# Performance work log

Measured on AMD Instinct MI355X. Metric: run time of the kernel, lower is better.

Reference implementation:

```python
import jax, jax.numpy as jnp
import numpy as np

N = 50000       # nodes
E = 800000      # edges (avg degree 16)
C_IN = 128
C_HID = 64
C_OUT = 64
NEG_SLOPE = 0.2  # PyG GATConv default


def setup_inputs() -> dict:
    key = jax.random.key(0)
    ks = jax.random.split(key, 20)
    inp = {
        "x": jax.random.normal(ks[0], (N, C_IN), dtype=jnp.float32),
        "edge_index": jax.random.randint(ks[1], (2, E), 0, N, dtype=jnp.int32),
        "batch_size": N,
        "framework": 1,
    }
    dims = [(C_IN, C_HID), (C_HID, C_HID), (C_HID, C_OUT)]
    k = 2
    for i, (cin, cout) in enumerate(dims):
        s = 1.0 / np.sqrt(cin)
        inp[f"W{i}"] = jax.random.normal(ks[k], (cin, cout), jnp.float32) * s; k += 1
        inp[f"a_src{i}"] = jax.random.normal(ks[k], (cout,), jnp.float32) * (1.0 / np.sqrt(cout)); k += 1
        inp[f"a_dst{i}"] = jax.random.normal(ks[k], (cout,), jnp.float32) * (1.0 / np.sqrt(cout)); k += 1
        inp[f"b{i}"] = jnp.zeros((cout,), jnp.float32); k += 1
    return inp


def _gat_conv(h, src, dst, n, W, a_src, a_dst, b):
    # h: [n, cin] -> [n, cout]; single head, PyG GATConv semantics
    hp = h @ W                                   # [n, cout]
    alpha_s = hp @ a_src                         # [n]
    alpha_d = hp @ a_dst                         # [n]
    e = alpha_s[src] + alpha_d[dst]              # [E'] per-edge logits
    e = jnp.where(e > 0, e, NEG_SLOPE * e)       # leaky_relu(0.2)
    # segment softmax over incoming edges of each destination node
    m = jax.ops.segment_max(e, dst, num_segments=n)
    e = jnp.exp(e - m[dst])
    denom = jax.ops.segment_sum(e, dst, num_segments=n)
    a = e / (denom[dst] + 1e-16)                 # [E']
    msg = hp[src] * a[:, None]                   # [E', cout]
    out = jax.ops.segment_sum(msg, dst, num_segments=n)
    return out + b


def reference(x, edge_index, batch_size, framework,
              W0, a_src0, a_dst0, b0,
              W1, a_src1, a_dst1, b1,
              W2, a_src2, a_dst2, b2):
    n = x.shape[0]
    loops = jnp.arange(n, dtype=edge_index.dtype)  # PyG add_self_loops=True
    src = jnp.concatenate([edge_index[0], loops])
    dst = jnp.concatenate([edge_index[1], loops])
    params = [(W0, a_src0, a_dst0, b0), (W1, a_src1, a_dst1, b1), (W2, a_src2, a_dst2, b2)]
    h = x
    for W, a_s, a_d, b in params:
        h = jax.nn.relu(_gat_conv(h, src, dst, n, W, a_s, a_d, b))
    if framework:
        return h
    return h[:batch_size]
```

## Files before the change

kernel.cpp:

```cpp
#include <hip/hip_runtime.h>
#include <hip/hip_fp16.h>
#include <math.h>

#define NEG_SLOPE 0.2f
#define BSHIFT 8
#define BCAP 8192

typedef __attribute__((ext_vector_type(8))) short bf16x8;
typedef __attribute__((ext_vector_type(4))) float f32x4;

__device__ __forceinline__ float leaky(float e) {
    return e > 0.f ? e : NEG_SLOPE * e;
}
__device__ __forceinline__ float to_f(float x) { return x; }
__device__ __forceinline__ float to_f(__half x) { return __half2float(x); }


__global__ __launch_bounds__(256) void partition_kernel(
        const int* __restrict__ src, const int* __restrict__ dst,
        int* __restrict__ bucketLen, int* __restrict__ pairs, int E, int nbk) {
    __shared__ int cnt[256];
    __shared__ int run[256];
    int t = threadIdx.x;
    int chunk = (E + gridDim.x - 1) / gridDim.x;
    int beg = blockIdx.x * chunk;
    int end = min(beg + chunk, E);
    cnt[t] = 0;
    __syncthreads();
    for (int i = beg + t; i < end; i += 256)
        atomicAdd(&cnt[dst[i] >> BSHIFT], 1);
    __syncthreads();
    if (t < nbk) run[t] = t * BCAP + atomicAdd(&bucketLen[t], cnt[t]);
    __syncthreads();
    for (int i = beg + t; i < end; i += 256) {
        int d = dst[i];
        int slot = atomicAdd(&run[d >> BSHIFT], 1);
        if (slot < (d >> BSHIFT) * BCAP + BCAP)
            pairs[slot] = (src[i] << BSHIFT) | (d & 255);
    }
}

__device__ void csr_build_body(
        int b, const int* __restrict__ bucketLen, const int* __restrict__ pairs,
        int* __restrict__ off, int* __restrict__ degA,
        int* __restrict__ csr_src, int N) {
    __shared__ int degl[256];
    __shared__ int s[256];
    __shared__ int cur[256];
    int t = threadIdx.x;
    int n0 = b << BSHIFT;
    int nodecnt = min(256, N - n0);
    int ebeg = b * BCAP;
    int eend = ebeg + bucketLen[b];

    degl[t] = 0;
    __syncthreads();
    for (int i = ebeg + t; i < eend; i += 256)
        atomicAdd(&degl[pairs[i] & 255], 1);
    __syncthreads();

    int v = degl[t];
    s[t] = v;
    __syncthreads();
    for (int o = 1; o < 256; o <<= 1) {
        int x = (t >= o) ? s[t - o] : 0;
        __syncthreads();
        s[t] += x;
        __syncthreads();
    }
    int excl = s[t] - v;
    if (t < nodecnt) {
        off[n0 + t] = ebeg + excl;
        degA[n0 + t] = v;
    }
    cur[t] = excl;
    __syncthreads();

    for (int i = ebeg + t; i < eend; i += 256) {
        int pk = pairs[i];
        int p = atomicAdd(&cur[pk & 255], 1);
        csr_src[ebeg + p] = pk >> BSHIFT;
    }
}


__device__ __forceinline__ unsigned f2bf_bits(float x) {
    unsigned u = __float_as_uint(x);
    return (u + 0x7fffu + ((u >> 16) & 1u)) >> 16;
}

__global__ __launch_bounds__(256) void pack_w3_kernel(
        const float* __restrict__ W0, const float* __restrict__ W1,
        const float* __restrict__ W2, short* __restrict__ Whi,
        short* __restrict__ Wlo, int* __restrict__ bucketLen) {
    int idx = blockIdx.x * 256 + threadIdx.x;
    if (idx < 256) bucketLen[idx] = 0;
    if (idx >= 16384) return;
    const float* W;
    int base, li;
    if (idx < 8192)       { W = W0; base = 0;     li = idx; }
    else if (idx < 12288) { W = W1; base = 8192;  li = idx - 8192; }
    else                  { W = W2; base = 12288; li = idx - 12288; }
    int k = li >> 6, col = li & 63;
    int c = k >> 5, kin = k & 31;
    int g = col >> 4, nn = col & 15;
    float x = W[li];
    unsigned hb = f2bf_bits(x);
    float hf = __uint_as_float(hb << 16);
    unsigned lb = f2bf_bits(x - hf);
    int o = base + (((c * 4 + g) * 16 + nn) << 5) + kin;
    Whi[o] = (short)hb;
    Wlo[o] = (short)lb;
}


template <int CIN, typename InT>
__device__ void gemm_body(
        int bid, const InT* __restrict__ h, const short* __restrict__ Whi,
        const short* __restrict__ Wlo,
        const float* __restrict__ a_src, const float* __restrict__ a_dst,
        __half* __restrict__ hp, float* __restrict__ as_, float* __restrict__ ad_,
        int n) {
    constexpr int KC = CIN / 32;
    int t = threadIdx.x, wave = t >> 6, lane = t & 63;
    int quad = lane >> 4, l16 = lane & 15;
    int node0 = bid * 64 + wave * 16;

    f32x4 acc[4];
#pragma unroll
    for (int g = 0; g < 4; ++g) acc[g] = (f32x4){0.f, 0.f, 0.f, 0.f};

    int nodeA = node0 + l16;
    bool va = nodeA < n;
    const InT* hrow = h + (size_t)(va ? nodeA : 0) * CIN + quad * 8;

#pragma unroll
    for (int c = 0; c < KC; ++c) {
        bf16x8 bhi[4], blo[4];
#pragma unroll
        for (int g = 0; g < 4; ++g) {
            int o = (((c * 4 + g) * 16 + l16) << 5) + quad * 8;
            bhi[g] = *(const bf16x8*)(Whi + o);
            blo[g] = *(const bf16x8*)(Wlo + o);
        }
        bf16x8 ahi, alo;
#pragma unroll
        for (int j = 0; j < 8; ++j) {
            float x = va ? to_f(hrow[c * 32 + j]) : 0.f;
            unsigned hb = f2bf_bits(x);
            float hf = __uint_as_float(hb << 16);
            unsigned lb = f2bf_bits(x - hf);
            ahi[j] = (short)hb;
            alo[j] = (short)lb;
        }
#pragma unroll
        for (int g = 0; g < 4; ++g) {
            acc[g] = __builtin_amdgcn_mfma_f32_16x16x32_bf16(ahi, bhi[g], acc[g], 0, 0, 0);
            acc[g] = __builtin_amdgcn_mfma_f32_16x16x32_bf16(ahi, blo[g], acc[g], 0, 0, 0);
            acc[g] = __builtin_amdgcn_mfma_f32_16x16x32_bf16(alo, bhi[g], acc[g], 0, 0, 0);
        }
    }

    float as4[4], ad4[4];
#pragma unroll
    for (int g = 0; g < 4; ++g) {
        as4[g] = a_src[g * 16 + l16];
        ad4[g] = a_dst[g * 16 + l16];
    }
#pragma unroll
    for (int r = 0; r < 4; ++r) {
        int node = node0 + quad * 4 + r;
        bool v = node < n;
        float vs = 0.f, vd = 0.f;
#pragma unroll
        for (int g = 0; g < 4; ++g) {
            float val = acc[g][r];
            if (v) hp[(size_t)node * 64 + g * 16 + l16] = __float2half_rn(val);
            vs = fmaf(val, as4[g], vs);
            vd = fmaf(val, ad4[g], vd);
        }
#pragma unroll
        for (int o = 1; o <= 8; o <<= 1) {
            vs += __shfl_xor(vs, o);
            vd += __shfl_xor(vd, o);
        }
        if (v && l16 == 0) {
            as_[node] = vs;
            ad_[node] = vd;
        }
    }
}

__global__ __launch_bounds__(256) void csr_gemm0_kernel(
        const int* __restrict__ bucketLen, const int* __restrict__ pairs,
        int* __restrict__ off, int* __restrict__ degA, int* __restrict__ csr_src,
        int N, int nbk,
        const float* __restrict__ x, const short* __restrict__ Whi,
        const short* __restrict__ Wlo, const float* __restrict__ a_src,
        const float* __restrict__ a_dst, __half* __restrict__ hp,
        float* __restrict__ as_, float* __restrict__ ad_) {
    if ((int)blockIdx.x < nbk)
        csr_build_body(blockIdx.x, bucketLen, pairs, off, degA, csr_src, N);
    else
        gemm_body<128, float>((int)blockIdx.x - nbk, x, Whi, Wlo, a_src, a_dst,
                              hp, as_, ad_, N);
}

template <int CIN, typename InT>
__global__ __launch_bounds__(256) void gemm_mfma_kernel(
        const InT* __restrict__ h, const short* __restrict__ Whi,
        const short* __restrict__ Wlo,
        const float* __restrict__ a_src, const float* __restrict__ a_dst,
        __half* __restrict__ hp, float* __restrict__ as_, float* __restrict__ ad_,
        int n) {
    gemm_body<CIN, InT>((int)blockIdx.x, h, Whi, Wlo, a_src, a_dst, hp, as_, ad_, n);
}


__device__ __forceinline__ void h4_to_f(uint2 u, float* f) {
    __half2 a = *(__half2*)&u.x;
    __half2 b = *(__half2*)&u.y;
    float2 f01 = __half22float2(a);
    float2 f23 = __half22float2(b);
    f[0] = f01.x; f[1] = f01.y; f[2] = f23.x; f[3] = f23.y;
}

__device__ __forceinline__ void store_row(float* out, size_t idx, float4 r) {
    ((float4*)out)[idx] = r;
}
__device__ __forceinline__ void store_row(__half* out, size_t idx, float4 r) {
    __half2 a = __floats2half2_rn(r.x, r.y);
    __half2 b = __floats2half2_rn(r.z, r.w);
    uint2 u;
    u.x = *(unsigned*)&a;
    u.y = *(unsigned*)&b;
    ((uint2*)out)[idx] = u;
}
__device__ __forceinline__ void store_el(float* out, size_t idx, float v) { out[idx] = v; }
__device__ __forceinline__ void store_el(__half* out, size_t idx, float v) { out[idx] = __float2half_rn(v); }

template <typename OutT>
__global__ __launch_bounds__(256) void agg_kernel(
        const __half* __restrict__ hp,
        const float* __restrict__ as_, const float* __restrict__ ad_,
        const int* __restrict__ off, const int* __restrict__ degA,
        const int* __restrict__ csr_src,
        const float* __restrict__ bias, OutT* __restrict__ out, int n) {
    __shared__ float pw[4][64];
    __shared__ int ps[4][64];
    int t = threadIdx.x;
    int wave = t >> 6, lane = t & 63;
    int hf = lane >> 5, l32 = lane & 31;
    int node = blockIdx.x * 8 + wave * 2 + hf;
    if (node >= n) return;

    int beg = off[node];
    int deg = degA[node];
    int end = beg + deg;
    float adst = ad_[node];
    float e_self = leaky(as_[node] + adst);

    if (deg <= 32) {
        bool valid = l32 < deg;
        int s = valid ? csr_src[beg + l32] : 0;
        float e = valid ? leaky(as_[s] + adst) : -3.4e38f;

        float m = e;
#pragma unroll
        for (int o = 16; o > 0; o >>= 1) m = fmaxf(m, __shfl_xor(m, o));
        m = fmaxf(m, e_self);

        float p = valid ? __expf(e - m) : 0.f;
        float pself = __expf(e_self - m);
        float se = p;
#pragma unroll
        for (int o = 16; o > 0; o >>= 1) se += __shfl_xor(se, o);
        se += pself;
        float inv = 1.0f / (se + 1e-16f);
        p *= inv;

        pw[wave][lane] = p;
        ps[wave][lane] = s;

        int group = l32 >> 4, sub = l32 & 15;
        const uint2* hp2 = (const uint2*)hp;

        float wself = (group == 0) ? pself * inv : 0.f;
        float hv[4];
        h4_to_f(hp2[(size_t)node * 16 + sub], hv);
        float ax = wself * hv[0], ay = wself * hv[1];
        float az = wself * hv[2], aw = wself * hv[3];

        int base = hf * 32;
        for (int j = group; j < deg; j += 8) {
            float w4[4];
            uint2 u4[4];
#pragma unroll
            for (int q = 0; q < 4; ++q) {
                int jj = j + 2 * q;
                bool ok = jj < deg;
                w4[q] = ok ? pw[wave][base + jj] : 0.f;
                u4[q] = ok ? hp2[(size_t)ps[wave][base + jj] * 16 + sub]
                           : make_uint2(0u, 0u);
            }
#pragma unroll
            for (int q = 0; q < 4; ++q) {
                float f[4];
                h4_to_f(u4[q], f);
                ax = fmaf(w4[q], f[0], ax);
                ay = fmaf(w4[q], f[1], ay);
                az = fmaf(w4[q], f[2], az);
                aw = fmaf(w4[q], f[3], aw);
            }
        }

        ax += __shfl_xor(ax, 16);
        ay += __shfl_xor(ay, 16);
        az += __shfl_xor(az, 16);
        aw += __shfl_xor(aw, 16);

        float4 b4 = ((const float4*)bias)[sub];
        float4 r;
        r.x = ax + b4.x; r.x = r.x > 0.f ? r.x : 0.f;
        r.y = ay + b4.y; r.y = r.y > 0.f ? r.y : 0.f;
        r.z = az + b4.z; r.z = r.z > 0.f ? r.z : 0.f;
        r.w = aw + b4.w; r.w = r.w > 0.f ? r.w : 0.f;
        if (group == 0) store_row(out, (size_t)node * 16 + sub, r);
    } else {
        float mymax = e_self;
        for (int i = beg + l32; i < end; i += 32) {
            int s = csr_src[i];
            mymax = fmaxf(mymax, leaky(as_[s] + adst));
        }
#pragma unroll
        for (int o = 16; o > 0; o >>= 1) mymax = fmaxf(mymax, __shfl_xor(mymax, o));
        float m = mymax;

        float se = 0.f;
        for (int i = beg + l32; i < end; i += 32) {
            int s = csr_src[i];
            se += __expf(leaky(as_[s] + adst) - m);
        }
#pragma unroll
        for (int o = 16; o > 0; o >>= 1) se += __shfl_xor(se, o);
        se += __expf(e_self - m);
        float inv = 1.0f / (se + 1e-16f);

        const __half2* hpx = (const __half2*)hp;
        float2 hs = __half22float2(hpx[(size_t)node * 32 + l32]);
        float wself = __expf(e_self - m) * inv;
        float a0 = wself * hs.x, a1 = wself * hs.y;
        for (int i = beg; i < end; ++i) {
            int s = csr_src[i];
            float w = __expf(leaky(as_[s] + adst) - m) * inv;
            float2 hv = __half22float2(hpx[(size_t)s * 32 + l32]);
            a0 = fmaf(w, hv.x, a0);
            a1 = fmaf(w, hv.y, a1);
        }
        float r0 = a0 + bias[l32 * 2];
        float r1 = a1 + bias[l32 * 2 + 1];
        store_el(out, (size_t)node * 64 + l32 * 2,     r0 > 0.f ? r0 : 0.f);
        store_el(out, (size_t)node * 64 + l32 * 2 + 1, r1 > 0.f ? r1 : 0.f);
    }
}


extern "C" void kernel_launch(void* const* d_in, const int* in_sizes, int n_in,
                              void* d_out, int out_size, void* d_ws, size_t ws_size,
                              hipStream_t stream) {
    const float* x = (const float*)d_in[0];
    const int* edge_index = (const int*)d_in[1];
    const int N = in_sizes[0] / 128;
    const int E = in_sizes[1] / 2;
    const int NBK = (N + 255) >> BSHIFT;

    const float* W[3]    = {(const float*)d_in[4], (const float*)d_in[8],  (const float*)d_in[12]};
    const float* asrc[3] = {(const float*)d_in[5], (const float*)d_in[9],  (const float*)d_in[13]};
    const float* adst[3] = {(const float*)d_in[6], (const float*)d_in[10], (const float*)d_in[14]};
    const float* bias[3] = {(const float*)d_in[7], (const float*)d_in[11], (const float*)d_in[15]};

    char* ws = (char*)d_ws;
    size_t o = 0;
    auto alloc = [&](size_t bytes) {
        char* p = ws + o;
        o += (bytes + 255) & ~(size_t)255;
        return p;
    };
    int* bucketLen    = (int*)alloc(256 * 4);
    int* pairs        = (int*)alloc((size_t)NBK * BCAP * 4);
    int* off          = (int*)alloc((size_t)N * 4);
    int* degA         = (int*)alloc((size_t)N * 4);
    int* csr_src      = (int*)alloc((size_t)NBK * BCAP * 4);
    float* as_        = (float*)alloc((size_t)N * 4);
    float* ad_        = (float*)alloc((size_t)N * 4);
    __half* hpbuf     = (__half*)alloc((size_t)N * 64 * 2);
    __half* actB      = (__half*)alloc((size_t)N * 64 * 2);
    short* Whi        = (short*)alloc(16384 * 2);
    short* Wlo        = (short*)alloc(16384 * 2);

    const int* srcp = edge_index;
    const int* dstp = edge_index + E;

    int gb = (N + 63) / 64;
    int ab = (N + 7) / 8;

    pack_w3_kernel<<<64, 256, 0, stream>>>(W[0], W[1], W[2], Whi, Wlo, bucketLen);
    partition_kernel<<<1024, 256, 0, stream>>>(srcp, dstp, bucketLen, pairs, E, NBK);

    csr_gemm0_kernel<<<NBK + gb, 256, 0, stream>>>(
        bucketLen, pairs, off, degA, csr_src, N, NBK,
        x, Whi, Wlo, asrc[0], adst[0], hpbuf, as_, ad_);
    agg_kernel<__half><<<ab, 256, 0, stream>>>(
        hpbuf, as_, ad_, off, degA, csr_src, bias[0], actB, N);

    gemm_mfma_kernel<64, __half><<<gb, 256, 0, stream>>>(
        actB, Whi + 8192, Wlo + 8192, asrc[1], adst[1], hpbuf, as_, ad_, N);
    agg_kernel<__half><<<ab, 256, 0, stream>>>(
        hpbuf, as_, ad_, off, degA, csr_src, bias[1], actB, N);

    gemm_mfma_kernel<64, __half><<<gb, 256, 0, stream>>>(
        actB, Whi + 12288, Wlo + 12288, asrc[2], adst[2], hpbuf, as_, ad_, N);
    agg_kernel<float><<<ab, 256, 0, stream>>>(
        hpbuf, as_, ad_, off, degA, csr_src, bias[2], (float*)d_out, N);
}
```

Baseline: 273.0 us.

## Fuse all GAT stages into one cooperative persistent kernel with grid syncs

```diff
diff --git a/kernel.cpp b/kernel.cpp
--- a/kernel.cpp
+++ b/kernel.cpp
@@ -1,6 +1,9 @@
 #include <hip/hip_runtime.h>
 #include <hip/hip_fp16.h>
+#include <hip/hip_cooperative_groups.h>
 #include <math.h>
+
+namespace cg = cooperative_groups;
 
 #define NEG_SLOPE 0.2f
 #define BSHIFT 8
@@ -15,87 +18,16 @@
 __device__ __forceinline__ float to_f(float x) { return x; }
 __device__ __forceinline__ float to_f(__half x) { return __half2float(x); }
 
-
-__global__ __launch_bounds__(256) void partition_kernel(
-        const int* __restrict__ src, const int* __restrict__ dst,
-        int* __restrict__ bucketLen, int* __restrict__ pairs, int E, int nbk) {
-    __shared__ int cnt[256];
-    __shared__ int run[256];
-    int t = threadIdx.x;
-    int chunk = (E + gridDim.x - 1) / gridDim.x;
-    int beg = blockIdx.x * chunk;
-    int end = min(beg + chunk, E);
-    cnt[t] = 0;
-    __syncthreads();
-    for (int i = beg + t; i < end; i += 256)
-        atomicAdd(&cnt[dst[i] >> BSHIFT], 1);
-    __syncthreads();
-    if (t < nbk) run[t] = t * BCAP + atomicAdd(&bucketLen[t], cnt[t]);
-    __syncthreads();
-    for (int i = beg + t; i < end; i += 256) {
-        int d = dst[i];
-        int slot = atomicAdd(&run[d >> BSHIFT], 1);
-        if (slot < (d >> BSHIFT) * BCAP + BCAP)
-            pairs[slot] = (src[i] << BSHIFT) | (d & 255);
-    }
-}
-
-__device__ void csr_build_body(
-        int b, const int* __restrict__ bucketLen, const int* __restrict__ pairs,
-        int* __restrict__ off, int* __restrict__ degA,
-        int* __restrict__ csr_src, int N) {
-    __shared__ int degl[256];
-    __shared__ int s[256];
-    __shared__ int cur[256];
-    int t = threadIdx.x;
-    int n0 = b << BSHIFT;
-    int nodecnt = min(256, N - n0);
-    int ebeg = b * BCAP;
-    int eend = ebeg + bucketLen[b];
-
-    degl[t] = 0;
-    __syncthreads();
-    for (int i = ebeg + t; i < eend; i += 256)
-        atomicAdd(&degl[pairs[i] & 255], 1);
-    __syncthreads();
-
-    int v = degl[t];
-    s[t] = v;
-    __syncthreads();
-    for (int o = 1; o < 256; o <<= 1) {
-        int x = (t >= o) ? s[t - o] : 0;
-        __syncthreads();
-        s[t] += x;
-        __syncthreads();
-    }
-    int excl = s[t] - v;
-    if (t < nodecnt) {
-        off[n0 + t] = ebeg + excl;
-        degA[n0 + t] = v;
-    }
-    cur[t] = excl;
-    __syncthreads();
-
-    for (int i = ebeg + t; i < eend; i += 256) {
-        int pk = pairs[i];
-        int p = atomicAdd(&cur[pk & 255], 1);
-        csr_src[ebeg + p] = pk >> BSHIFT;
-    }
-}
-
-
 __device__ __forceinline__ unsigned f2bf_bits(float x) {
     unsigned u = __float_as_uint(x);
     return (u + 0x7fffu + ((u >> 16) & 1u)) >> 16;
 }
 
-__global__ __launch_bounds__(256) void pack_w3_kernel(
-        const float* __restrict__ W0, const float* __restrict__ W1,
+
+__device__ __forceinline__ void pack_body(
+        int idx, const float* __restrict__ W0, const float* __restrict__ W1,
         const float* __restrict__ W2, short* __restrict__ Whi,
-        short* __restrict__ Wlo, int* __restrict__ bucketLen) {
-    int idx = blockIdx.x * 256 + threadIdx.x;
-    if (idx < 256) bucketLen[idx] = 0;
-    if (idx >= 16384) return;
+        short* __restrict__ Wlo) {
     const float* W;
     int base, li;
     if (idx < 8192)       { W = W0; base = 0;     li = idx; }
@@ -114,6 +46,76 @@
 }
 
 
+__device__ void partition_body(
+        const int* __restrict__ src, const int* __restrict__ dst,
+        int* __restrict__ bucketLen, int* __restrict__ pairs, int E, int nbk) {
+    __shared__ int cnt[256];
+    __shared__ int run[256];
+    int t = threadIdx.x;
+    int nblk = gridDim.x;
+    int chunk = (E + nblk - 1) / nblk;
+    int beg = blockIdx.x * chunk;
+    int end = min(beg + chunk, E);
+    cnt[t] = 0;
+    __syncthreads();
+    for (int i = beg + t; i < end; i += 256)
+        atomicAdd(&cnt[dst[i] >> BSHIFT], 1);
+    __syncthreads();
+    if (t < nbk) run[t] = t * BCAP + atomicAdd(&bucketLen[t], cnt[t]);
+    __syncthreads();
+    for (int i = beg + t; i < end; i += 256) {
+        int d = dst[i];
+        int slot = atomicAdd(&run[d >> BSHIFT], 1);
+        if (slot < (d >> BSHIFT) * BCAP + BCAP)
+            pairs[slot] = (src[i] << BSHIFT) | (d & 255);
+    }
+}
+
+__device__ void csr_build_body(
+        int b, const int* __restrict__ bucketLen, const int* __restrict__ pairs,
+        int* __restrict__ off, int* __restrict__ degA,
+        int* __restrict__ csr_src, int N) {
+    __shared__ int degl[256];
+    __shared__ int s[256];
+    __shared__ int cur[256];
+    int t = threadIdx.x;
+    int n0 = b << BSHIFT;
+    int nodecnt = min(256, N - n0);
+    int ebeg = b * BCAP;
+    int eend = ebeg + bucketLen[b];
+
+    degl[t] = 0;
+    __syncthreads();
+    for (int i = ebeg + t; i < eend; i += 256)
+        atomicAdd(&degl[pairs[i] & 255], 1);
+    __syncthreads();
+
+    int v = degl[t];
+    s[t] = v;
+    __syncthreads();
+    for (int o = 1; o < 256; o <<= 1) {
+        int x = (t >= o) ? s[t - o] : 0;
+        __syncthreads();
+        s[t] += x;
+        __syncthreads();
+    }
+    int excl = s[t] - v;
+    if (t < nodecnt) {
+        off[n0 + t] = ebeg + excl;
+        degA[n0 + t] = v;
+    }
+    cur[t] = excl;
+    __syncthreads();
+
+    for (int i = ebeg + t; i < eend; i += 256) {
+        int pk = pairs[i];
+        int p = atomicAdd(&cur[pk & 255], 1);
+        csr_src[ebeg + p] = pk >> BSHIFT;
+    }
+    __syncthreads();
+}
+
+
 template <int CIN, typename InT>
 __device__ void gemm_body(
         int bid, const InT* __restrict__ h, const short* __restrict__ Whi,
@@ -189,6 +191,233 @@
             ad_[node] = vd;
         }
     }
+}
+
+
+__device__ __forceinline__ void h4_to_f(uint2 u, float* f) {
+    __half2 a = *(__half2*)&u.x;
+    __half2 b = *(__half2*)&u.y;
+    float2 f01 = __half22float2(a);
+    float2 f23 = __half22float2(b);
+    f[0] = f01.x; f[1] = f01.y; f[2] = f23.x; f[3] = f23.y;
+}
+
+__device__ __forceinline__ void store_row(float* out, size_t idx, float4 r) {
+    ((float4*)out)[idx] = r;
+}
+__device__ __forceinline__ void store_row(__half* out, size_t idx, float4 r) {
+    __half2 a = __floats2half2_rn(r.x, r.y);
+    __half2 b = __floats2half2_rn(r.z, r.w);
+    uint2 u;
+    u.x = *(unsigned*)&a;
+    u.y = *(unsigned*)&b;
+    ((uint2*)out)[idx] = u;
+}
+__device__ __forceinline__ void store_el(float* out, size_t idx, float v) { out[idx] = v; }
+__device__ __forceinline__ void store_el(__half* out, size_t idx, float v) { out[idx] = __float2half_rn(v); }
+
+template <typename OutT>
+__device__ void agg_body(
+        int g0, const __half* __restrict__ hp,
+        const float* __restrict__ as_, const float* __restrict__ ad_,
+        const int* __restrict__ off, const int* __restrict__ degA,
+        const int* __restrict__ csr_src,
+        const float* __restrict__ bias, OutT* __restrict__ out, int n) {
+    __shared__ float pw[4][64];
+    __shared__ int ps[4][64];
+    int t = threadIdx.x;
+    int wave = t >> 6, lane = t & 63;
+    int hf = lane >> 5, l32 = lane & 31;
+    int node = g0 * 8 + wave * 2 + hf;
+    if (node < n) {
+        int beg = off[node];
+        int deg = degA[node];
+        int end = beg + deg;
+        float adst = ad_[node];
+        float e_self = leaky(as_[node] + adst);
+
+        if (deg <= 32) {
+            bool valid = l32 < deg;
+            int s = valid ? csr_src[beg + l32] : 0;
+            float e = valid ? leaky(as_[s] + adst) : -3.4e38f;
+
+            float m = e;
+#pragma unroll
+            for (int o = 16; o > 0; o >>= 1) m = fmaxf(m, __shfl_xor(m, o));
+            m = fmaxf(m, e_self);
+
+            float p = valid ? __expf(e - m) : 0.f;
+            float pself = __expf(e_self - m);
+            float se = p;
+#pragma unroll
+            for (int o = 16; o > 0; o >>= 1) se += __shfl_xor(se, o);
+            se += pself;
+            float inv = 1.0f / (se + 1e-16f);
+            p *= inv;
+
+            pw[wave][lane] = p;
+            ps[wave][lane] = s;
+
+            int group = l32 >> 4, sub = l32 & 15;
+            const uint2* hp2 = (const uint2*)hp;
+
+            float wself = (group == 0) ? pself * inv : 0.f;
+            float hv[4];
+            h4_to_f(hp2[(size_t)node * 16 + sub], hv);
+            float ax = wself * hv[0], ay = wself * hv[1];
+            float az = wself * hv[2], aw = wself * hv[3];
+
+            int base = hf * 32;
+            for (int j = group; j < deg; j += 8) {
+                float w4[4];
+                uint2 u4[4];
+#pragma unroll
+                for (int q = 0; q < 4; ++q) {
+                    int jj = j + 2 * q;
+                    bool ok = jj < deg;
+                    w4[q] = ok ? pw[wave][base + jj] : 0.f;
+                    u4[q] = ok ? hp2[(size_t)ps[wave][base + jj] * 16 + sub]
+                               : make_uint2(0u, 0u);
+                }
+#pragma unroll
+                for (int q = 0; q < 4; ++q) {
+                    float f[4];
+                    h4_to_f(u4[q], f);
+                    ax = fmaf(w4[q], f[0], ax);
+                    ay = fmaf(w4[q], f[1], ay);
+                    az = fmaf(w4[q], f[2], az);
+                    aw = fmaf(w4[q], f[3], aw);
+                }
+            }
+
+            ax += __shfl_xor(ax, 16);
+            ay += __shfl_xor(ay, 16);
+            az += __shfl_xor(az, 16);
+            aw += __shfl_xor(aw, 16);
+
+            float4 b4 = ((const float4*)bias)[sub];
+            float4 r;
+            r.x = ax + b4.x; r.x = r.x > 0.f ? r.x : 0.f;
+            r.y = ay + b4.y; r.y = r.y > 0.f ? r.y : 0.f;
+            r.z = az + b4.z; r.z = r.z > 0.f ? r.z : 0.f;
+            r.w = aw + b4.w; r.w = r.w > 0.f ? r.w : 0.f;
+            if (group == 0) store_row(out, (size_t)node * 16 + sub, r);
+        } else {
+            float mymax = e_self;
+            for (int i = beg + l32; i < end; i += 32) {
+                int s = csr_src[i];
+                mymax = fmaxf(mymax, leaky(as_[s] + adst));
+            }
+#pragma unroll
+            for (int o = 16; o > 0; o >>= 1) mymax = fmaxf(mymax, __shfl_xor(mymax, o));
+            float m = mymax;
+
+            float se = 0.f;
+            for (int i = beg + l32; i < end; i += 32) {
+                int s = csr_src[i];
+                se += __expf(leaky(as_[s] + adst) - m);
+            }
+#pragma unroll
+            for (int o = 16; o > 0; o >>= 1) se += __shfl_xor(se, o);
+            se += __expf(e_self - m);
+            float inv = 1.0f / (se + 1e-16f);
+
+            const __half2* hpx = (const __half2*)hp;
+            float2 hs = __half22float2(hpx[(size_t)node * 32 + l32]);
+            float wself = __expf(e_self - m) * inv;
+            float a0 = wself * hs.x, a1 = wself * hs.y;
+            for (int i = beg; i < end; ++i) {
+                int s = csr_src[i];
+                float w = __expf(leaky(as_[s] + adst) - m) * inv;
+                float2 hv = __half22float2(hpx[(size_t)s * 32 + l32]);
+                a0 = fmaf(w, hv.x, a0);
+                a1 = fmaf(w, hv.y, a1);
+            }
+            float r0 = a0 + bias[l32 * 2];
+            float r1 = a1 + bias[l32 * 2 + 1];
+            store_el(out, (size_t)node * 64 + l32 * 2,     r0 > 0.f ? r0 : 0.f);
+            store_el(out, (size_t)node * 64 + l32 * 2 + 1, r1 > 0.f ? r1 : 0.f);
+        }
+    }
+}
+
+
+struct MegaArgs {
+    const float* x;
+    const int* src;
+    const int* dst;
+    const float* W0; const float* W1; const float* W2;
+    const float* as0; const float* ad0; const float* b0;
+    const float* as1; const float* ad1; const float* b1;
+    const float* as2; const float* ad2; const float* b2;
+    int* bucketLen; int* pairs; int* off; int* degA; int* csr_src;
+    float* asA; float* adA;
+    __half* hp; __half* actB;
+    short* Whi; short* Wlo;
+    float* out;
+    int N, E, NBK, GB, AB;
+};
+
+__global__ __launch_bounds__(256) void mega_kernel(MegaArgs a) {
+    cg::grid_group grid = cg::this_grid();
+    int bid = blockIdx.x, nblk = gridDim.x, t = threadIdx.x;
+
+    for (int idx = bid * 256 + t; idx < 16384; idx += nblk * 256)
+        pack_body(idx, a.W0, a.W1, a.W2, a.Whi, a.Wlo);
+    if (bid == 0) a.bucketLen[t] = 0;
+    grid.sync();
+
+    partition_body(a.src, a.dst, a.bucketLen, a.pairs, a.E, a.NBK);
+    grid.sync();
+
+    if (bid < a.NBK) {
+        csr_build_body(bid, a.bucketLen, a.pairs, a.off, a.degA, a.csr_src, a.N);
+    } else {
+        for (int tile = bid - a.NBK; tile < a.GB; tile += nblk - a.NBK)
+            gemm_body<128, float>(tile, a.x, a.Whi, a.Wlo, a.as0, a.ad0,
+                                  a.hp, a.asA, a.adA, a.N);
+    }
+    grid.sync();
+
+    for (int g = bid; g < a.AB; g += nblk)
+        agg_body<__half>(g, a.hp, a.asA, a.adA, a.off, a.degA, a.csr_src,
+                         a.b0, a.actB, a.N);
+    grid.sync();
+
+    for (int tile = bid; tile < a.GB; tile += nblk)
+        gemm_body<64, __half>(tile, a.actB, a.Whi + 8192, a.Wlo + 8192,
+                              a.as1, a.ad1, a.hp, a.asA, a.adA, a.N);
+    grid.sync();
+
+    for (int g = bid; g < a.AB; g += nblk)
+        agg_body<__half>(g, a.hp, a.asA, a.adA, a.off, a.degA, a.csr_src,
+                         a.b1, a.actB, a.N);
+    grid.sync();
+
+    for (int tile = bid; tile < a.GB; tile += nblk)
+        gemm_body<64, __half>(tile, a.actB, a.Whi + 12288, a.Wlo + 12288,
+                              a.as2, a.ad2, a.hp, a.asA, a.adA, a.N);
+    grid.sync();
+
+    for (int g = bid; g < a.AB; g += nblk)
+        agg_body<float>(g, a.hp, a.asA, a.adA, a.off, a.degA, a.csr_src,
+                        a.b2, a.out, a.N);
+}
+
+
+__global__ __launch_bounds__(256) void pack_w3_kernel(
+        const float* __restrict__ W0, const float* __restrict__ W1,
+        const float* __restrict__ W2, short* __restrict__ Whi,
+        short* __restrict__ Wlo, int* __restrict__ bucketLen) {
+    int idx = blockIdx.x * 256 + threadIdx.x;
+    if (idx < 256) bucketLen[idx] = 0;
+    if (idx < 16384) pack_body(idx, W0, W1, W2, Whi, Wlo);
+}
+
+__global__ __launch_bounds__(256) void partition_kernel(
+        const int* __restrict__ src, const int* __restrict__ dst,
+        int* __restrict__ bucketLen, int* __restrict__ pairs, int E, int nbk) {
+    partition_body(src, dst, bucketLen, pairs, E, nbk);
 }
 
 __global__ __launch_bounds__(256) void csr_gemm0_kernel(
@@ -216,29 +445,6 @@
     gemm_body<CIN, InT>((int)blockIdx.x, h, Whi, Wlo, a_src, a_dst, hp, as_, ad_, n);
 }
 
-
-__device__ __forceinline__ void h4_to_f(uint2 u, float* f) {
-    __half2 a = *(__half2*)&u.x;
-    __half2 b = *(__half2*)&u.y;
-    float2 f01 = __half22float2(a);
-    float2 f23 = __half22float2(b);
-    f[0] = f01.x; f[1] = f01.y; f[2] = f23.x; f[3] = f23.y;
-}
-
-__device__ __forceinline__ void store_row(float* out, size_t idx, float4 r) {
-    ((float4*)out)[idx] = r;
-}
-__device__ __forceinline__ void store_row(__half* out, size_t idx, float4 r) {
-    __half2 a = __floats2half2_rn(r.x, r.y);
-    __half2 b = __floats2half2_rn(r.z, r.w);
-    uint2 u;
-    u.x = *(unsigned*)&a;
-    u.y = *(unsigned*)&b;
-    ((uint2*)out)[idx] = u;
-}
-__device__ __forceinline__ void store_el(float* out, size_t idx, float v) { out[idx] = v; }
-__device__ __forceinline__ void store_el(__half* out, size_t idx, float v) { out[idx] = __float2half_rn(v); }
-
 template <typename OutT>
 __global__ __launch_bounds__(256) void agg_kernel(
         const __half* __restrict__ hp,
@@ -246,122 +452,7 @@
         const int* __restrict__ off, const int* __restrict__ degA,
         const int* __restrict__ csr_src,
         const float* __restrict__ bias, OutT* __restrict__ out, int n) {
-    __shared__ float pw[4][64];
-    __shared__ int ps[4][64];
-    int t = threadIdx.x;
-    int wave = t >> 6, lane = t & 63;
-    int hf = lane >> 5, l32 = lane & 31;
-    int node = blockIdx.x * 8 + wave * 2 + hf;
-    if (node >= n) return;
-
-    int beg = off[node];
-    int deg = degA[node];
-    int end = beg + deg;
-    float adst = ad_[node];
-    float e_self = leaky(as_[node] + adst);
-
-    if (deg <= 32) {
-        bool valid = l32 < deg;
-        int s = valid ? csr_src[beg + l32] : 0;
-        float e = valid ? leaky(as_[s] + adst) : -3.4e38f;
-
-        float m = e;
-#pragma unroll
-        for (int o = 16; o > 0; o >>= 1) m = fmaxf(m, __shfl_xor(m, o));
-        m = fmaxf(m, e_self);
-
-        float p = valid ? __expf(e - m) : 0.f;
-        float pself = __expf(e_self - m);
-        float se = p;
-#pragma unroll
-        for (int o = 16; o > 0; o >>= 1) se += __shfl_xor(se, o);
-        se += pself;
-        float inv = 1.0f / (se + 1e-16f);
-        p *= inv;
-
-        pw[wave][lane] = p;
-        ps[wave][lane] = s;
-
-        int group = l32 >> 4, sub = l32 & 15;
-        const uint2* hp2 = (const uint2*)hp;
-
-        float wself = (group == 0) ? pself * inv : 0.f;
-        float hv[4];
-        h4_to_f(hp2[(size_t)node * 16 + sub], hv);
-        float ax = wself * hv[0], ay = wself * hv[1];
-        float az = wself * hv[2], aw = wself * hv[3];
-
-        int base = hf * 32;
-        for (int j = group; j < deg; j += 8) {
-            float w4[4];
-            uint2 u4[4];
-#pragma unroll
-            for (int q = 0; q < 4; ++q) {
-                int jj = j + 2 * q;
-                bool ok = jj < deg;
-                w4[q] = ok ? pw[wave][base + jj] : 0.f;
-                u4[q] = ok ? hp2[(size_t)ps[wave][base + jj] * 16 + sub]
-                           : make_uint2(0u, 0u);
-            }
-#pragma unroll
-            for (int q = 0; q < 4; ++q) {
-                float f[4];
-                h4_to_f(u4[q], f);
-                ax = fmaf(w4[q], f[0], ax);
-                ay = fmaf(w4[q], f[1], ay);
-                az = fmaf(w4[q], f[2], az);
-                aw = fmaf(w4[q], f[3], aw);
-            }
-        }
-
-        ax += __shfl_xor(ax, 16);
-        ay += __shfl_xor(ay, 16);
-        az += __shfl_xor(az, 16);
-        aw += __shfl_xor(aw, 16);
-
-        float4 b4 = ((const float4*)bias)[sub];
-        float4 r;
-        r.x = ax + b4.x; r.x = r.x > 0.f ? r.x : 0.f;
-        r.y = ay + b4.y; r.y = r.y > 0.f ? r.y : 0.f;
-        r.z = az + b4.z; r.z = r.z > 0.f ? r.z : 0.f;
-        r.w = aw + b4.w; r.w = r.w > 0.f ? r.w : 0.f;
-        if (group == 0) store_row(out, (size_t)node * 16 + sub, r);
-    } else {
-        float mymax = e_self;
-        for (int i = beg + l32; i < end; i += 32) {
-            int s = csr_src[i];
-            mymax = fmaxf(mymax, leaky(as_[s] + adst));
-        }
-#pragma unroll
-        for (int o = 16; o > 0; o >>= 1) mymax = fmaxf(mymax, __shfl_xor(mymax, o));
-        float m = mymax;
-
-        float se = 0.f;
-        for (int i = beg + l32; i < end; i += 32) {
-            int s = csr_src[i];
-            se += __expf(leaky(as_[s] + adst) - m);
-        }
-#pragma unroll
-        for (int o = 16; o > 0; o >>= 1) se += __shfl_xor(se, o);
-        se += __expf(e_self - m);
-        float inv = 1.0f / (se + 1e-16f);
-
-        const __half2* hpx = (const __half2*)hp;
-        float2 hs = __half22float2(hpx[(size_t)node * 32 + l32]);
-        float wself = __expf(e_self - m) * inv;
-        float a0 = wself * hs.x, a1 = wself * hs.y;
-        for (int i = beg; i < end; ++i) {
-            int s = csr_src[i];
-            float w = __expf(leaky(as_[s] + adst) - m) * inv;
-            float2 hv = __half22float2(hpx[(size_t)s * 32 + l32]);
-            a0 = fmaf(w, hv.x, a0);
-            a1 = fmaf(w, hv.y, a1);
-        }
-        float r0 = a0 + bias[l32 * 2];
-        float r1 = a1 + bias[l32 * 2 + 1];
-        store_el(out, (size_t)node * 64 + l32 * 2,     r0 > 0.f ? r0 : 0.f);
-        store_el(out, (size_t)node * 64 + l32 * 2 + 1, r1 > 0.f ? r1 : 0.f);
-    }
+    agg_body<OutT>((int)blockIdx.x, hp, as_, ad_, off, degA, csr_src, bias, out, n);
 }
 
 
@@ -404,22 +495,68 @@
     int gb = (N + 63) / 64;
     int ab = (N + 7) / 8;
 
-    pack_w3_kernel<<<64, 256, 0, stream>>>(W[0], W[1], W[2], Whi, Wlo, bucketLen);
-    partition_kernel<<<1024, 256, 0, stream>>>(srcp, dstp, bucketLen, pairs, E, NBK);
-
-    csr_gemm0_kernel<<<NBK + gb, 256, 0, stream>>>(
-        bucketLen, pairs, off, degA, csr_src, N, NBK,
-        x, Whi, Wlo, asrc[0], adst[0], hpbuf, as_, ad_);
-    agg_kernel<__half><<<ab, 256, 0, stream>>>(
-        hpbuf, as_, ad_, off, degA, csr_src, bias[0], actB, N);
-
-    gemm_mfma_kernel<64, __half><<<gb, 256, 0, stream>>>(
-        actB, Whi + 8192, Wlo + 8192, asrc[1], adst[1], hpbuf, as_, ad_, N);
-    agg_kernel<__half><<<ab, 256, 0, stream>>>(
-        hpbuf, as_, ad_, off, degA, csr_src, bias[1], actB, N);
-
-    gemm_mfma_kernel<64, __half><<<gb, 256, 0, stream>>>(
-        actB, Whi + 12288, Wlo + 12288, asrc[2], adst[2], hpbuf, as_, ad_, N);
-    agg_kernel<float><<<ab, 256, 0, stream>>>(
-        hpbuf, as_, ad_, off, degA, csr_src, bias[2], (float*)d_out, N);
-}
+    static int s_blocks = 0;
+    static bool s_coop_ok = true;
+    if (s_coop_ok && s_blocks == 0) {
+        int dev = 0;
+        hipDeviceProp_t prop;
+        if (hipGetDevice(&dev) == hipSuccess &&
+            hipGetDeviceProperties(&prop, dev) == hipSuccess &&
+            prop.cooperativeLaunch) {
+            int maxPerCU = 0;
+            if (hipOccupancyMaxActiveBlocksPerMultiprocessor(
+                    &maxPerCU, mega_kernel, 256, 0) == hipSuccess && maxPerCU > 0) {
+                long b = (long)prop.multiProcessorCount * (long)maxPerCU;
+                if (b > 4096) b = 4096;
+                s_blocks = (int)b;
+            } else {
+                s_coop_ok = false;
+            }
+        } else {
+            s_coop_ok = false;
+        }
+    }
+
+    bool launched = false;
+    if (s_coop_ok && s_blocks > NBK) {
+        MegaArgs a;
+        a.x = x; a.src = srcp; a.dst = dstp;
+        a.W0 = W[0]; a.W1 = W[1]; a.W2 = W[2];
+        a.as0 = asrc[0]; a.ad0 = adst[0]; a.b0 = bias[0];
+        a.as1 = asrc[1]; a.ad1 = adst[1]; a.b1 = bias[1];
+        a.as2 = asrc[2]; a.ad2 = adst[2]; a.b2 = bias[2];
+        a.bucketLen = bucketLen; a.pairs = pairs; a.off = off;
+        a.degA = degA; a.csr_src = csr_src;
+        a.asA = as_; a.adA = ad_;
+        a.hp = hpbuf; a.actB = actB;
+        a.Whi = Whi; a.Wlo = Wlo;
+        a.out = (float*)d_out;
+        a.N = N; a.E = E; a.NBK = NBK; a.GB = gb; a.AB = ab;
+        void* params[] = { (void*)&a };
+        hipError_t err = hipLaunchCooperativeKernel(
+            mega_kernel, dim3(s_blocks), dim3(256), params, 0u, stream);
+        if (err == hipSuccess) {
+            launched = true;
+        } else {
+            s_coop_ok = false;
+        }
+    }
+
+    if (!launched) {
+        pack_w3_kernel<<<64, 256, 0, stream>>>(W[0], W[1], W[2], Whi, Wlo, bucketLen);
+        partition_kernel<<<1024, 256, 0, stream>>>(srcp, dstp, bucketLen, pairs, E, NBK);
+        csr_gemm0_kernel<<<NBK + gb, 256, 0, stream>>>(
+            bucketLen, pairs, off, degA, csr_src, N, NBK,
+            x, Whi, Wlo, asrc[0], adst[0], hpbuf, as_, ad_);
+        agg_kernel<__half><<<ab, 256, 0, stream>>>(
+            hpbuf, as_, ad_, off, degA, csr_src, bias[0], actB, N);
+        gemm_mfma_kernel<64, __half><<<gb, 256, 0, stream>>>(
+            actB, Whi + 8192, Wlo + 8192, asrc[1], adst[1], hpbuf, as_, ad_, N);
+        agg_kernel<__half><<<ab, 256, 0, stream>>>(
+            hpbuf, as_, ad_, off, degA, csr_src, bias[1], actB, N);
+        gemm_mfma_kernel<64, __half><<<gb, 256, 0, stream>>>(
+            actB, Whi + 12288, Wlo + 12288, asrc[2], adst[2], hpbuf, as_, ad_, N);
+        agg_kernel<float><<<ab, 256, 0, stream>>>(
+            hpbuf, as_, ad_, off, degA, csr_src, bias[2], (float*)d_out, N);
+    }
+}
```

Measured after the change: 790.0 us. +189.4%, slower.

## Fuse aggregation of layer i with GEMM of layer i+1 via LDS tile

Applied to the files above, without the earlier changes.

```diff
diff --git a/kernel.cpp b/kernel.cpp
--- a/kernel.cpp
+++ b/kernel.cpp
@@ -15,79 +15,11 @@
 __device__ __forceinline__ float to_f(float x) { return x; }
 __device__ __forceinline__ float to_f(__half x) { return __half2float(x); }
 
-
-__global__ __launch_bounds__(256) void partition_kernel(
-        const int* __restrict__ src, const int* __restrict__ dst,
-        int* __restrict__ bucketLen, int* __restrict__ pairs, int E, int nbk) {
-    __shared__ int cnt[256];
-    __shared__ int run[256];
-    int t = threadIdx.x;
-    int chunk = (E + gridDim.x - 1) / gridDim.x;
-    int beg = blockIdx.x * chunk;
-    int end = min(beg + chunk, E);
-    cnt[t] = 0;
-    __syncthreads();
-    for (int i = beg + t; i < end; i += 256)
-        atomicAdd(&cnt[dst[i] >> BSHIFT], 1);
-    __syncthreads();
-    if (t < nbk) run[t] = t * BCAP + atomicAdd(&bucketLen[t], cnt[t]);
-    __syncthreads();
-    for (int i = beg + t; i < end; i += 256) {
-        int d = dst[i];
-        int slot = atomicAdd(&run[d >> BSHIFT], 1);
-        if (slot < (d >> BSHIFT) * BCAP + BCAP)
-            pairs[slot] = (src[i] << BSHIFT) | (d & 255);
-    }
-}
-
-__device__ void csr_build_body(
-        int b, const int* __restrict__ bucketLen, const int* __restrict__ pairs,
-        int* __restrict__ off, int* __restrict__ degA,
-        int* __restrict__ csr_src, int N) {
-    __shared__ int degl[256];
-    __shared__ int s[256];
-    __shared__ int cur[256];
-    int t = threadIdx.x;
-    int n0 = b << BSHIFT;
-    int nodecnt = min(256, N - n0);
-    int ebeg = b * BCAP;
-    int eend = ebeg + bucketLen[b];
-
-    degl[t] = 0;
-    __syncthreads();
-    for (int i = ebeg + t; i < eend; i += 256)
-        atomicAdd(&degl[pairs[i] & 255], 1);
-    __syncthreads();
-
-    int v = degl[t];
-    s[t] = v;
-    __syncthreads();
-    for (int o = 1; o < 256; o <<= 1) {
-        int x = (t >= o) ? s[t - o] : 0;
-        __syncthreads();
-        s[t] += x;
-        __syncthreads();
-    }
-    int excl = s[t] - v;
-    if (t < nodecnt) {
-        off[n0 + t] = ebeg + excl;
-        degA[n0 + t] = v;
-    }
-    cur[t] = excl;
-    __syncthreads();
-
-    for (int i = ebeg + t; i < eend; i += 256) {
-        int pk = pairs[i];
-        int p = atomicAdd(&cur[pk & 255], 1);
-        csr_src[ebeg + p] = pk >> BSHIFT;
-    }
-}
-
-
 __device__ __forceinline__ unsigned f2bf_bits(float x) {
     unsigned u = __float_as_uint(x);
     return (u + 0x7fffu + ((u >> 16) & 1u)) >> 16;
 }
+
 
 __global__ __launch_bounds__(256) void pack_w3_kernel(
         const float* __restrict__ W0, const float* __restrict__ W1,
@@ -114,7 +46,75 @@
 }
 
 
-template <int CIN, typename InT>
+__global__ __launch_bounds__(256) void partition_kernel(
+        const int* __restrict__ src, const int* __restrict__ dst,
+        int* __restrict__ bucketLen, int* __restrict__ pairs, int E, int nbk) {
+    __shared__ int cnt[256];
+    __shared__ int run[256];
+    int t = threadIdx.x;
+    int chunk = (E + gridDim.x - 1) / gridDim.x;
+    int beg = blockIdx.x * chunk;
+    int end = min(beg + chunk, E);
+    cnt[t] = 0;
+    __syncthreads();
+    for (int i = beg + t; i < end; i += 256)
+        atomicAdd(&cnt[dst[i] >> BSHIFT], 1);
+    __syncthreads();
+    if (t < nbk) run[t] = t * BCAP + atomicAdd(&bucketLen[t], cnt[t]);
+    __syncthreads();
+    for (int i = beg + t; i < end; i += 256) {
+        int d = dst[i];
+        int slot = atomicAdd(&run[d >> BSHIFT], 1);
+        if (slot < (d >> BSHIFT) * BCAP + BCAP)
+            pairs[slot] = (src[i] << BSHIFT) | (d & 255);
+    }
+}
+
+__device__ void csr_build_body(
+        int b, const int* __restrict__ bucketLen, const int* __restrict__ pairs,
+        int* __restrict__ off, int* __restrict__ degA,
+        int* __restrict__ csr_src, int N) {
+    __shared__ int degl[256];
+    __shared__ int s[256];
+    __shared__ int cur[256];
+    int t = threadIdx.x;
+    int n0 = b << BSHIFT;
+    int nodecnt = min(256, N - n0);
+    int ebeg = b * BCAP;
+    int eend = ebeg + bucketLen[b];
+
+    degl[t] = 0;
+    __syncthreads();
+    for (int i = ebeg + t; i < eend; i += 256)
+        atomicAdd(&degl[pairs[i] & 255], 1);
+    __syncthreads();
+
+    int v = degl[t];
+    s[t] = v;
+    __syncthreads();
+    for (int o = 1; o < 256; o <<= 1) {
+        int x = (t >= o) ? s[t - o] : 0;
+        __syncthreads();
+        s[t] += x;
+        __syncthreads();
+    }
+    int excl = s[t] - v;
+    if (t < nodecnt) {
+        off[n0 + t] = ebeg + excl;
+        degA[n0 + t] = v;
+    }
+    cur[t] = excl;
+    __syncthreads();
+
+    for (int i = ebeg + t; i < eend; i += 256) {
+        int pk = pairs[i];
+        int p = atomicAdd(&cur[pk & 255], 1);
+        csr_src[ebeg + p] = pk >> BSHIFT;
+    }
+}
+
+
+template <int CIN, typename InT, bool LOCAL>
 __device__ void gemm_body(
         int bid, const InT* __restrict__ h, const short* __restrict__ Whi,
         const short* __restrict__ Wlo,
@@ -132,7 +132,8 @@
 
     int nodeA = node0 + l16;
     bool va = nodeA < n;
-    const InT* hrow = h + (size_t)(va ? nodeA : 0) * CIN + quad * 8;
+    int rowA = LOCAL ? (wave * 16 + l16) : (va ? nodeA : 0);
+    const InT* hrow = h + (size_t)rowA * CIN + quad * 8;
 
 #pragma unroll
     for (int c = 0; c < KC; ++c) {
@@ -190,6 +191,181 @@
         }
     }
 }
+
+
+__device__ __forceinline__ void h4_to_f(uint2 u, float* f) {
+    __half2 a = *(__half2*)&u.x;
+    __half2 b = *(__half2*)&u.y;
+    float2 f01 = __half22float2(a);
+    float2 f23 = __half22float2(b);
+    f[0] = f01.x; f[1] = f01.y; f[2] = f23.x; f[3] = f23.y;
+}
+
+__device__ __forceinline__ void store_row(float* out, size_t idx, float4 r) {
+    ((float4*)out)[idx] = r;
+}
+__device__ __forceinline__ void store_row(__half* out, size_t idx, float4 r) {
+    __half2 a = __floats2half2_rn(r.x, r.y);
+    __half2 b = __floats2half2_rn(r.z, r.w);
+    uint2 u;
+    u.x = *(unsigned*)&a;
+    u.y = *(unsigned*)&b;
+    ((uint2*)out)[idx] = u;
+}
+__device__ __forceinline__ void store_el(float* out, size_t idx, float v) { out[idx] = v; }
+__device__ __forceinline__ void store_el(__half* out, size_t idx, float v) { out[idx] = __float2half_rn(v); }
+
+template <typename OutT>
+__device__ void agg_body(
+        int node, int store_node, const __half* __restrict__ hp,
+        const float* __restrict__ as_, const float* __restrict__ ad_,
+        const int* __restrict__ off, const int* __restrict__ degA,
+        const int* __restrict__ csr_src,
+        const float* __restrict__ bias, OutT* __restrict__ out, int n) {
+    __shared__ float pw[4][64];
+    __shared__ int ps[4][64];
+    int t = threadIdx.x;
+    int wave = t >> 6, lane = t & 63;
+    int hf = lane >> 5, l32 = lane & 31;
+    if (node >= n) return;
+
+    int beg = off[node];
+    int deg = degA[node];
+    int end = beg + deg;
+    float adst = ad_[node];
+    float e_self = leaky(as_[node] + adst);
+
+    if (deg <= 32) {
+        bool valid = l32 < deg;
+        int s = valid ? csr_src[beg + l32] : 0;
+        float e = valid ? leaky(as_[s] + adst) : -3.4e38f;
+
+        float m = e;
+#pragma unroll
+        for (int o = 16; o > 0; o >>= 1) m = fmaxf(m, __shfl_xor(m, o));
+        m = fmaxf(m, e_self);
+
+        float p = valid ? __expf(e - m) : 0.f;
+        float pself = __expf(e_self - m);
+        float se = p;
+#pragma unroll
+        for (int o = 16; o > 0; o >>= 1) se += __shfl_xor(se, o);
+        se += pself;
+        float inv = 1.0f / (se + 1e-16f);
+        p *= inv;
+
+        pw[wave][lane] = p;
+        ps[wave][lane] = s;
+
+        int group = l32 >> 4, sub = l32 & 15;
+        const uint2* hp2 = (const uint2*)hp;
+
+        float wself = (group == 0) ? pself * inv : 0.f;
+        float hv[4];
+        h4_to_f(hp2[(size_t)node * 16 + sub], hv);
+        float ax = wself * hv[0], ay = wself * hv[1];
+        float az = wself * hv[2], aw = wself * hv[3];
+
+        int base = hf * 32;
+        for (int j = group; j < deg; j += 8) {
+            float w4[4];
+            uint2 u4[4];
+#pragma unroll
+            for (int q = 0; q < 4; ++q) {
+                int jj = j + 2 * q;
+                bool ok = jj < deg;
+                w4[q] = ok ? pw[wave][base + jj] : 0.f;
+                u4[q] = ok ? hp2[(size_t)ps[wave][base + jj] * 16 + sub]
+                           : make_uint2(0u, 0u);
+            }
+#pragma unroll
+            for (int q = 0; q < 4; ++q) {
+                float f[4];
+                h4_to_f(u4[q], f);
+                ax = fmaf(w4[q], f[0], ax);
+                ay = fmaf(w4[q], f[1], ay);
+                az = fmaf(w4[q], f[2], az);
+                aw = fmaf(w4[q], f[3], aw);
+            }
+        }
+
+        ax += __shfl_xor(ax, 16);
+        ay += __shfl_xor(ay, 16);
+        az += __shfl_xor(az, 16);
+        aw += __shfl_xor(aw, 16);
+
+        float4 b4 = ((const float4*)bias)[sub];
+        float4 r;
+        r.x = ax + b4.x; r.x = r.x > 0.f ? r.x : 0.f;
+        r.y = ay + b4.y; r.y = r.y > 0.f ? r.y : 0.f;
+        r.z = az + b4.z; r.z = r.z > 0.f ? r.z : 0.f;
+        r.w = aw + b4.w; r.w = r.w > 0.f ? r.w : 0.f;
+        if (group == 0) store_row(out, (size_t)store_node * 16 + sub, r);
+    } else {
+        float mymax = e_self;
+        for (int i = beg + l32; i < end; i += 32) {
+            int s = csr_src[i];
+            mymax = fmaxf(mymax, leaky(as_[s] + adst));
+        }
+#pragma unroll
+        for (int o = 16; o > 0; o >>= 1) mymax = fmaxf(mymax, __shfl_xor(mymax, o));
+        float m = mymax;
+
+        float se = 0.f;
+        for (int i = beg + l32; i < end; i += 32) {
+            int s = csr_src[i];
+            se += __expf(leaky(as_[s] + adst) - m);
+        }
+#pragma unroll
+        for (int o = 16; o > 0; o >>= 1) se += __shfl_xor(se, o);
+        se += __expf(e_self - m);
+        float inv = 1.0f / (se + 1e-16f);
+
+        const __half2* hpx = (const __half2*)hp;
+        float2 hs = __half22float2(hpx[(size_t)node * 32 + l32]);
+        float wself = __expf(e_self - m) * inv;
+        float a0 = wself * hs.x, a1 = wself * hs.y;
+        for (int i = beg; i < end; ++i) {
+            int s = csr_src[i];
+            float w = __expf(leaky(as_[s] + adst) - m) * inv;
+            float2 hv = __half22float2(hpx[(size_t)s * 32 + l32]);
+            a0 = fmaf(w, hv.x, a0);
+            a1 = fmaf(w, hv.y, a1);
+        }
+        float r0 = a0 + bias[l32 * 2];
+        float r1 = a1 + bias[l32 * 2 + 1];
+        store_el(out, (size_t)store_node * 64 + l32 * 2,     r0 > 0.f ? r0 : 0.f);
+        store_el(out, (size_t)store_node * 64 + l32 * 2 + 1, r1 > 0.f ? r1 : 0.f);
+    }
+}
+
+
+__global__ __launch_bounds__(256) void fused_agg_gemm_kernel(
+        const __half* __restrict__ hp_in,
+        const float* __restrict__ as_in, const float* __restrict__ ad_in,
+        const int* __restrict__ off, const int* __restrict__ degA,
+        const int* __restrict__ csr_src, const float* __restrict__ bias_i,
+        const short* __restrict__ Whi, const short* __restrict__ Wlo,
+        const float* __restrict__ a_src, const float* __restrict__ a_dst,
+        __half* __restrict__ hp_out, float* __restrict__ as_out,
+        float* __restrict__ ad_out, int n) {
+    __shared__ __half actT[64 * 64];
+    int t = threadIdx.x, wave = t >> 6, lane = t & 63;
+    int hf = lane >> 5;
+    int base = blockIdx.x * 64;
+
+#pragma unroll 1
+    for (int k = 0; k < 8; ++k) {
+        int local = k * 8 + wave * 2 + hf;
+        agg_body<__half>(base + local, local, hp_in, as_in, ad_in,
+                         off, degA, csr_src, bias_i, actT, n);
+    }
+    __syncthreads();
+
+    gemm_body<64, __half, true>(blockIdx.x, actT, Whi, Wlo, a_src, a_dst,
+                                hp_out, as_out, ad_out, n);
+}
+
 
 __global__ __launch_bounds__(256) void csr_gemm0_kernel(
         const int* __restrict__ bucketLen, const int* __restrict__ pairs,
@@ -202,42 +378,9 @@
     if ((int)blockIdx.x < nbk)
         csr_build_body(blockIdx.x, bucketLen, pairs, off, degA, csr_src, N);
     else
-        gemm_body<128, float>((int)blockIdx.x - nbk, x, Whi, Wlo, a_src, a_dst,
-                              hp, as_, ad_, N);
-}
-
-template <int CIN, typename InT>
-__global__ __launch_bounds__(256) void gemm_mfma_kernel(
-        const InT* __restrict__ h, const short* __restrict__ Whi,
-        const short* __restrict__ Wlo,
-        const float* __restrict__ a_src, const float* __restrict__ a_dst,
-        __half* __restrict__ hp, float* __restrict__ as_, float* __restrict__ ad_,
-        int n) {
-    gemm_body<CIN, InT>((int)blockIdx.x, h, Whi, Wlo, a_src, a_dst, hp, as_, ad_, n);
-}
-
-
-__device__ __forceinline__ void h4_to_f(uint2 u, float* f) {
-    __half2 a = *(__half2*)&u.x;
-    __half2 b = *(__half2*)&u.y;
-    float2 f01 = __half22float2(a);
-    float2 f23 = __half22float2(b);
-    f[0] = f01.x; f[1] = f01.y; f[2] = f23.x; f[3] = f23.y;
-}
-
-__device__ __forceinline__ void store_row(float* out, size_t idx, float4 r) {
-    ((float4*)out)[idx] = r;
-}
-__device__ __forceinline__ void store_row(__half* out, size_t idx, float4 r) {
-    __half2 a = __floats2half2_rn(r.x, r.y);
-    __half2 b = __floats2half2_rn(r.z, r.w);
-    uint2 u;
-    u.x = *(unsigned*)&a;
-    u.y = *(unsigned*)&b;
-    ((uint2*)out)[idx] = u;
-}
-__device__ __forceinline__ void store_el(float* out, size_t idx, float v) { out[idx] = v; }
-__device__ __forceinline__ void store_el(__half* out, size_t idx, float v) { out[idx] = __float2half_rn(v); }
+        gemm_body<128, float, false>((int)blockIdx.x - nbk, x, Whi, Wlo,
+                                     a_src, a_dst, hp, as_, ad_, N);
+}
 
 template <typename OutT>
 __global__ __launch_bounds__(256) void agg_kernel(
@@ -246,122 +389,11 @@
         const int* __restrict__ off, const int* __restrict__ degA,
         const int* __restrict__ csr_src,
         const float* __restrict__ bias, OutT* __restrict__ out, int n) {
-    __shared__ float pw[4][64];
-    __shared__ int ps[4][64];
     int t = threadIdx.x;
     int wave = t >> 6, lane = t & 63;
-    int hf = lane >> 5, l32 = lane & 31;
+    int hf = lane >> 5;
     int node = blockIdx.x * 8 + wave * 2 + hf;
-    if (node >= n) return;
-
-    int beg = off[node];
-    int deg = degA[node];
-    int end = beg + deg;
-    float adst = ad_[node];
-    float e_self = leaky(as_[node] + adst);
-
-    if (deg <= 32) {
-        bool valid = l32 < deg;
-        int s = valid ? csr_src[beg + l32] : 0;
-        float e = valid ? leaky(as_[s] + adst) : -3.4e38f;
-
-        float m = e;
-#pragma unroll
-        for (int o = 16; o > 0; o >>= 1) m = fmaxf(m, __shfl_xor(m, o));
-        m = fmaxf(m, e_self);
-
-        float p = valid ? __expf(e - m) : 0.f;
-        float pself = __expf(e_self - m);
-        float se = p;
-#pragma unroll
-        for (int o = 16; o > 0; o >>= 1) se += __shfl_xor(se, o);
-        se += pself;
-        float inv = 1.0f / (se + 1e-16f);
-        p *= inv;
-
-        pw[wave][lane] = p;
-        ps[wave][lane] = s;
-
-        int group = l32 >> 4, sub = l32 & 15;
-        const uint2* hp2 = (const uint2*)hp;
-
-        float wself = (group == 0) ? pself * inv : 0.f;
-        float hv[4];
-        h4_to_f(hp2[(size_t)node * 16 + sub], hv);
-        float ax = wself * hv[0], ay = wself * hv[1];
-        float az = wself * hv[2], aw = wself * hv[3];
-
-        int base = hf * 32;
-        for (int j = group; j < deg; j += 8) {
-            float w4[4];
-            uint2 u4[4];
-#pragma unroll
-            for (int q = 0; q < 4; ++q) {
-                int jj = j + 2 * q;
-                bool ok = jj < deg;
-                w4[q] = ok ? pw[wave][base + jj] : 0.f;
-                u4[q] = ok ? hp2[(size_t)ps[wave][base + jj] * 16 + sub]
-                           : make_uint2(0u, 0u);
-            }
-#pragma unroll
-            for (int q = 0; q < 4; ++q) {
-                float f[4];
-                h4_to_f(u4[q], f);
-                ax = fmaf(w4[q], f[0], ax);
-                ay = fmaf(w4[q], f[1], ay);
-                az = fmaf(w4[q], f[2], az);
-                aw = fmaf(w4[q], f[3], aw);
-            }
-        }
-
-        ax += __shfl_xor(ax, 16);
-        ay += __shfl_xor(ay, 16);
-        az += __shfl_xor(az, 16);
-        aw += __shfl_xor(aw, 16);
-
-        float4 b4 = ((const float4*)bias)[sub];
-        float4 r;
-        r.x = ax + b4.x; r.x = r.x > 0.f ? r.x : 0.f;
-        r.y = ay + b4.y; r.y = r.y > 0.f ? r.y : 0.f;
-        r.z = az + b4.z; r.z = r.z > 0.f ? r.z : 0.f;
-        r.w = aw + b4.w; r.w = r.w > 0.f ? r.w : 0.f;
-        if (group == 0) store_row(out, (size_t)node * 16 + sub, r);
-    } else {
-        float mymax = e_self;
-        for (int i = beg + l32; i < end; i += 32) {
-            int s = csr_src[i];
-            mymax = fmaxf(mymax, leaky(as_[s] + adst));
-        }
-#pragma unroll
-        for (int o = 16; o > 0; o >>= 1) mymax = fmaxf(mymax, __shfl_xor(mymax, o));
-        float m = mymax;
-
-        float se = 0.f;
-        for (int i = beg + l32; i < end; i += 32) {
-            int s = csr_src[i];
-            se += __expf(leaky(as_[s] + adst) - m);
-        }
-#pragma unroll
-        for (int o = 16; o > 0; o >>= 1) se += __shfl_xor(se, o);
-        se += __expf(e_self - m);
-        float inv = 1.0f / (se + 1e-16f);
-
-        const __half2* hpx = (const __half2*)hp;
-        float2 hs = __half22float2(hpx[(size_t)node * 32 + l32]);
-        float wself = __expf(e_self - m) * inv;
-        float a0 = wself * hs.x, a1 = wself * hs.y;
-        for (int i = beg; i < end; ++i) {
-            int s = csr_src[i];
-            float w = __expf(leaky(as_[s] + adst) - m) * inv;
-            float2 hv = __half22float2(hpx[(size_t)s * 32 + l32]);
-            a0 = fmaf(w, hv.x, a0);
-            a1 = fmaf(w, hv.y, a1);
-        }
-        float r0 = a0 + bias[l32 * 2];
-        float r1 = a1 + bias[l32 * 2 + 1];
-        store_el(out, (size_t)node * 64 + l32 * 2,     r0 > 0.f ? r0 : 0.f);
-        store_el(out, (size_t)node * 64 + l32 * 2 + 1, r1 > 0.f ? r1 : 0.f);
-    }
+    agg_body<OutT>(node, node, hp, as_, ad_, off, degA, csr_src, bias, out, n);
 }
 
 
@@ -391,10 +423,12 @@
     int* off          = (int*)alloc((size_t)N * 4);
     int* degA         = (int*)alloc((size_t)N * 4);
     int* csr_src      = (int*)alloc((size_t)NBK * BCAP * 4);
-    float* as_        = (float*)alloc((size_t)N * 4);
-    float* ad_        = (float*)alloc((size_t)N * 4);
-    __half* hpbuf     = (__half*)alloc((size_t)N * 64 * 2);
-    __half* actB      = (__half*)alloc((size_t)N * 64 * 2);
+    float* asA        = (float*)alloc((size_t)N * 4);
+    float* adA        = (float*)alloc((size_t)N * 4);
+    float* asB        = (float*)alloc((size_t)N * 4);
+    float* adB        = (float*)alloc((size_t)N * 4);
+    __half* hpA       = (__half*)alloc((size_t)N * 64 * 2);
+    __half* hpB       = (__half*)alloc((size_t)N * 64 * 2);
     short* Whi        = (short*)alloc(16384 * 2);
     short* Wlo        = (short*)alloc(16384 * 2);
 
@@ -409,17 +443,16 @@
 
     csr_gemm0_kernel<<<NBK + gb, 256, 0, stream>>>(
         bucketLen, pairs, off, degA, csr_src, N, NBK,
-        x, Whi, Wlo, asrc[0], adst[0], hpbuf, as_, ad_);
-    agg_kernel<__half><<<ab, 256, 0, stream>>>(
-        hpbuf, as_, ad_, off, degA, csr_src, bias[0], actB, N);
-
-    gemm_mfma_kernel<64, __half><<<gb, 256, 0, stream>>>(
-        actB, Whi + 8192, Wlo + 8192, asrc[1], adst[1], hpbuf, as_, ad_, N);
-    agg_kernel<__half><<<ab, 256, 0, stream>>>(
-        hpbuf, as_, ad_, off, degA, csr_src, bias[1], actB, N);
-
-    gemm_mfma_kernel<64, __half><<<gb, 256, 0, stream>>>(
-        actB, Whi + 12288, Wlo + 12288, asrc[2], adst[2], hpbuf, as_, ad_, N);
+        x, Whi, Wlo, asrc[0], adst[0], hpA, asA, adA);
+
+    fused_agg_gemm_kernel<<<gb, 256, 0, stream>>>(
+        hpA, asA, adA, off, degA, csr_src, bias[0],
+        Whi + 8192, Wlo + 8192, asrc[1], adst[1], hpB, asB, adB, N);
+
+    fused_agg_gemm_kernel<<<gb, 256, 0, stream>>>(
+        hpB, asB, adB, off, degA, csr_src, bias[1],
+        Whi + 12288, Wlo + 12288, asrc[2], adst[2], hpA, asA, adA, N);
+
     agg_kernel<float><<<ab, 256, 0, stream>>>(
-        hpbuf, as_, ad_, off, degA, csr_src, bias[2], (float*)d_out, N);
-}
+        hpA, asA, adA, off, degA, csr_src, bias[2], (float*)d_out, N);
+}
```

After: 274.5 us. Within noise of the previous version (+0.6%).
